# Optimization experiments

Hardware: AMD Instinct MI355X
Metric: run time of the kernel (lower is better)

Reference implementation:

```python
import jax, jax.numpy as jnp
import numpy as np

B = 4096      # batch
D_IN = 512    # input_dim
D = 256       # d_model
T = 424       # n_targets
L = 6         # num_layers
EPS = 1e-5    # torch LayerNorm default


def _ln(x, g, b):
    m = jnp.mean(x, axis=-1, keepdims=True)
    v = jnp.var(x, axis=-1, keepdims=True)
    return (x - m) * jax.lax.rsqrt(v + EPS) * g + b


def setup_inputs() -> dict:
    key = jax.random.key(0)
    ks = iter(jax.random.split(key, 32))
    r = lambda shape, s=0.05: jax.random.normal(next(ks), shape, dtype=jnp.float32) * s
    return {
        'x': jax.random.normal(next(ks), (B, D_IN), dtype=jnp.float32),
        'proj_W': r((4, D // 4, D_IN)), 'proj_b': r((4, D // 4)),
        'attn_in_W': r((L, 3 * D, D)), 'attn_in_b': r((L, 3 * D)),
        'attn_out_W': r((L, D, D)), 'attn_out_b': r((L, D)),
        'ln_g': jnp.ones((L, D), jnp.float32), 'ln_b': jnp.zeros((L, D), jnp.float32),
        'ff_W1': r((L, 4 * D, D)), 'ff_b1': r((L, 4 * D)),
        'ff_W2': r((L, D, 4 * D)), 'ff_b2': r((L, D)),
        'cross_in_W': r((3 * D, D)), 'cross_in_b': r((3 * D,)),
        'cross_out_W': r((D, D)), 'cross_out_b': r((D,)),
        'tp_W1': r((T, D // 2, D)), 'tp_b1': r((T, D // 2)),
        'tp_ln_g': jnp.ones((T, D // 2), jnp.float32), 'tp_ln_b': jnp.zeros((T, D // 2), jnp.float32),
        'tp_W2': r((T, D // 4, D // 2)), 'tp_b2': r((T, D // 4)),
        'tp_W3': r((T, D // 4)), 'tp_b3': r((T,)),
    }


def reference(x, proj_W, proj_b, attn_in_W, attn_in_b, attn_out_W, attn_out_b,
              ln_g, ln_b, ff_W1, ff_b1, ff_W2, ff_b2,
              cross_in_W, cross_in_b, cross_out_W, cross_out_b,
              tp_W1, tp_b1, tp_ln_g, tp_ln_b, tp_W2, tp_b2, tp_W3, tp_b3):
    # 4 feature projections -> concat == reshape of stacked einsum  [B, 4, D/4] -> [B, D]
    h = jnp.einsum('bd,pkd->bpk', x, proj_W) + proj_b
    h = h.reshape(h.shape[0], D)

    # 6 transformer blocks on seq_len=1: softmax over a single key == 1, so
    # MHA(x,x,x) reduces exactly to out_proj(v_proj(x)); dropout = identity (eval).
    for i in range(L):
        Wv, bv = attn_in_W[i, 2 * D:], attn_in_b[i, 2 * D:]
        attn = (h @ Wv.T + bv) @ attn_out_W[i].T + attn_out_b[i]
        h = _ln(h + attn, ln_g[i], ln_b[i])          # same norm instance reused
        ff = jax.nn.gelu(h @ ff_W1[i].T + ff_b1[i], approximate=False) @ ff_W2[i].T + ff_b2[i]
        h = _ln(h + ff, ln_g[i], ln_b[i])

    # cross-target attention, also seq_len=1 -> v/out projections only
    Wv, bv = cross_in_W[2 * D:], cross_in_b[2 * D:]
    h = h + ((h @ Wv.T + bv) @ cross_out_W.T + cross_out_b)

    # 424 per-target MLP heads, batched as grouped GEMMs
    t = jnp.einsum('bd,tkd->btk', h, tp_W1) + tp_b1          # [B, T, 128]
    t = jax.nn.relu(_ln(t, tp_ln_g, tp_ln_b))
    t = jax.nn.relu(jnp.einsum('btk,tmk->btm', t, tp_W2) + tp_b2)  # [B, T, 64]
    out = jnp.einsum('btm,tm->bt', t, tp_W3) + tp_b3         # [B, T]
    return out
```

## Files before the change

### kernel.cpp

```cpp
#include <hip/hip_runtime.h>
#include <stdint.h>

using bf16x8 = __attribute__((ext_vector_type(8))) short;
using f32x4  = __attribute__((ext_vector_type(4))) float;

__device__ __forceinline__ f32x4 mfma16(bf16x8 a, bf16x8 b, f32x4 c) {
  return __builtin_amdgcn_mfma_f32_16x16x32_bf16(a, b, c, 0, 0, 0);
}

__device__ __forceinline__ unsigned short f2b_rne(float f) {
  union { float f; unsigned u; } v; v.f = f;
  unsigned r = v.u + 0x7fffu + ((v.u >> 16) & 1u);
  return (unsigned short)(r >> 16);
}

__global__ void f2b_kernel(const float* __restrict__ s, unsigned short* __restrict__ d, int n4) {
  int i = blockIdx.x * 256 + threadIdx.x;
  if (i >= n4) return;
  float4 v = reinterpret_cast<const float4*>(s)[i];
  ushort4 o;
  o.x = f2b_rne(v.x); o.y = f2b_rne(v.y); o.z = f2b_rne(v.z); o.w = f2b_rne(v.w);
  reinterpret_cast<ushort4*>(d)[i] = o;
}

__global__ __launch_bounds__(256) void compose_attn(
    const float* __restrict__ aiW, const float* __restrict__ aib,
    const float* __restrict__ aoW, const float* __restrict__ aob,
    const float* __restrict__ ciW, const float* __restrict__ cib,
    const float* __restrict__ coW, const float* __restrict__ cob,
    unsigned short* __restrict__ wEff, float* __restrict__ bEff) {
  const int mat = blockIdx.y;
  const float* Wo = (mat < 6) ? aoW + (size_t)mat * 65536 : coW;
  const float* Wv = (mat < 6) ? aiW + (size_t)mat * 196608 + 131072 : ciW + 131072;
  const float* bv = (mat < 6) ? aib + mat * 768 + 512 : cib + 512;
  const float* bo = (mat < 6) ? aob + mat * 256 : cob;
  unsigned short* Wd = wEff + (size_t)mat * 65536;
  const int m = blockIdx.x * 16 + (threadIdx.x >> 4);
  const int k0 = (threadIdx.x & 15) * 16;
  float c[16] = {};
  for (int j = 0; j < 256; ++j) {
    const float a = Wo[m * 256 + j];
    const float* Br = Wv + j * 256 + k0;
#pragma unroll
    for (int kk = 0; kk < 16; ++kk) c[kk] = fmaf(a, Br[kk], c[kk]);
  }
#pragma unroll
  for (int kk = 0; kk < 16; ++kk) Wd[m * 256 + k0 + kk] = f2b_rne(c[kk]);
  if (blockIdx.x == 0) {
    const int mm = threadIdx.x;
    float s = 0.f;
    for (int j = 0; j < 256; ++j) s = fmaf(Wo[mm * 256 + j], bv[j], s);
    bEff[mat * 256 + mm] = s + bo[mm];
  }
}

template<int NCF, int K, int NK>
__device__ __forceinline__ void gemm_ws(const unsigned short* __restrict__ Wb,
                                        const char* __restrict__ smA_r,
                                        int hi16, int swz, f32x4 (&acc)[NCF]) {
  bf16x8 w[3][NCF];
#pragma unroll
  for (int p = 0; p < 2; ++p)
#pragma unroll
    for (int cf = 0; cf < NCF; ++cf)
      w[p][cf] = *reinterpret_cast<const bf16x8*>(Wb + (size_t)cf * 16 * K + p * 32);
#pragma unroll
  for (int ks = 0; ks < NK; ++ks) {
    const bf16x8 a = *reinterpret_cast<const bf16x8*>(smA_r + ((ks * 64 + hi16) ^ swz));
    if (ks + 2 < NK) {
#pragma unroll
      for (int cf = 0; cf < NCF; ++cf)
        w[(ks + 2) % 3][cf] = *reinterpret_cast<const bf16x8*>(Wb + (size_t)cf * 16 * K + (ks + 2) * 32);
    }
#pragma unroll
    for (int cf = 0; cf < NCF; ++cf)
      acc[cf] = mfma16(a, w[ks % 3][cf], acc[cf]);
  }
}

__global__ __launch_bounds__(512, 2) void trunk_fused(
    const unsigned short* __restrict__ xb, const unsigned short* __restrict__ pWb,
    const float* __restrict__ projb,
    const unsigned short* __restrict__ wEff, const float* __restrict__ bEff,
    const unsigned short* __restrict__ f1Wb, const float* __restrict__ f1b,
    const unsigned short* __restrict__ f2Wb, const float* __restrict__ f2bp,
    const float* __restrict__ lng, const float* __restrict__ lnb,
    unsigned short* __restrict__ hbf) {
  __shared__ char hbuf[16 * 512];
  __shared__ char gbuf[16 * 2048];
  __shared__ float red[2][16][8];
  const int tid = threadIdx.x, wid = tid >> 6, lane = tid & 63;
  const int r = lane & 15, hi = lane >> 4;
  const int swz = (r & 7) << 4, hi16 = hi * 16;
  const int row0 = blockIdx.x << 4;
  const int colb = wid * 32;

#pragma unroll
  for (int i = 0; i < 2; ++i) {
    const int id = tid + i * 512, row = id >> 6, c8 = id & 63;
    bf16x8 v = *reinterpret_cast<const bf16x8*>(xb + (size_t)(row0 + row) * 512 + c8 * 8);
    *reinterpret_cast<bf16x8*>(gbuf + row * 1024 + ((c8 * 16) ^ ((row & 7) << 4))) = v;
  }
  __syncthreads();

  f32x4 hreg[2];

  auto store_hb = [&]() {
#pragma unroll
    for (int cf = 0; cf < 2; ++cf) {
      const int cb = (colb + cf * 16 + r) * 2;
#pragma unroll
      for (int j = 0; j < 4; ++j) {
        const int row = hi * 4 + j;
        *reinterpret_cast<unsigned short*>(hbuf + row * 512 + (cb ^ ((row & 7) << 4))) =
            f2b_rne(hreg[cf][j]);
      }
    }
  };

  auto ln_apply = [&](float gm0, float gm1, float bb0, float bb1) {
    float sum[4], sq[4];
#pragma unroll
    for (int j = 0; j < 4; ++j) {
      const float v0 = hreg[0][j], v1 = hreg[1][j];
      sum[j] = v0 + v1; sq[j] = v0 * v0 + v1 * v1;
    }
#pragma unroll
    for (int m = 1; m < 16; m <<= 1)
#pragma unroll
      for (int j = 0; j < 4; ++j) {
        sum[j] += __shfl_xor(sum[j], m, 64);
        sq[j]  += __shfl_xor(sq[j],  m, 64);
      }
    if (r == 0)
#pragma unroll
      for (int j = 0; j < 4; ++j) {
        red[0][hi * 4 + j][wid] = sum[j];
        red[1][hi * 4 + j][wid] = sq[j];
      }
    __syncthreads();
#pragma unroll
    for (int j = 0; j < 4; ++j) {
      const int row = hi * 4 + j;
      f32x4 p0 = *reinterpret_cast<const f32x4*>(&red[0][row][0]);
      f32x4 p1 = *reinterpret_cast<const f32x4*>(&red[0][row][4]);
      f32x4 q0 = *reinterpret_cast<const f32x4*>(&red[1][row][0]);
      f32x4 q1 = *reinterpret_cast<const f32x4*>(&red[1][row][4]);
      const float ts = p0[0]+p0[1]+p0[2]+p0[3]+p1[0]+p1[1]+p1[2]+p1[3];
      const float tq = q0[0]+q0[1]+q0[2]+q0[3]+q1[0]+q1[1]+q1[2]+q1[3];
      const float mean = ts * (1.f / 256.f);
      const float rstd = rsqrtf(tq * (1.f / 256.f) - mean * mean + 1e-5f);
      hreg[0][j] = (hreg[0][j] - mean) * rstd * gm0 + bb0;
      hreg[1][j] = (hreg[1][j] - mean) * rstd * gm1 + bb1;
    }
  };

  {
    f32x4 acc[2] = {};
    gemm_ws<2, 512, 16>(pWb + (size_t)(colb + r) * 512 + hi * 8, gbuf + r * 1024, hi16, swz, acc);
    const float bv0 = projb[colb + r], bv1 = projb[colb + 16 + r];
#pragma unroll
    for (int j = 0; j < 4; ++j) { hreg[0][j] = acc[0][j] + bv0; hreg[1][j] = acc[1][j] + bv1; }
  }
  store_hb();
  __syncthreads();

  for (int L = 0; L < 6; ++L) {
    const float gm0 = lng[L * 256 + colb + r],      gm1 = lng[L * 256 + colb + 16 + r];
    const float bb0 = lnb[L * 256 + colb + r],      bb1 = lnb[L * 256 + colb + 16 + r];
    {
      f32x4 acc[2] = {};
      gemm_ws<2, 256, 8>(wEff + (size_t)L * 65536 + (size_t)(colb + r) * 256 + hi * 8,
                         hbuf + r * 512, hi16, swz, acc);
      const float be0 = bEff[L * 256 + colb + r], be1 = bEff[L * 256 + colb + 16 + r];
#pragma unroll
      for (int j = 0; j < 4; ++j) { hreg[0][j] += acc[0][j] + be0; hreg[1][j] += acc[1][j] + be1; }
    }
    ln_apply(gm0, gm1, bb0, bb1);
    store_hb();
    __syncthreads();
    {
      f32x4 accf[8] = {};
      gemm_ws<8, 256, 8>(f1Wb + (size_t)L * 262144 + (size_t)(wid * 128 + r) * 256 + hi * 8,
                         hbuf + r * 512, hi16, swz, accf);
#pragma unroll
      for (int cf = 0; cf < 8; ++cf) {
        const int colw = wid * 128 + cf * 16 + r;
        const float bv = f1b[L * 1024 + colw];
        const int cb = colw * 2;
#pragma unroll
        for (int j = 0; j < 4; ++j) {
          float y = accf[cf][j] + bv;
          y = 0.5f * y * (1.f + erff(y * 0.70710678118654752f));
          const int row = hi * 4 + j;
          *reinterpret_cast<unsigned short*>(gbuf + row * 2048 + (cb ^ ((row & 7) << 4))) = f2b_rne(y);
        }
      }
    }
    __syncthreads();
    {
      f32x4 acc[2] = {};
      gemm_ws<2, 1024, 32>(f2Wb + (size_t)L * 262144 + (size_t)(colb + r) * 1024 + hi * 8,
                           gbuf + r * 2048, hi16, swz, acc);
      const float be0 = f2bp[L * 256 + colb + r], be1 = f2bp[L * 256 + colb + 16 + r];
#pragma unroll
      for (int j = 0; j < 4; ++j) { hreg[0][j] += acc[0][j] + be0; hreg[1][j] += acc[1][j] + be1; }
    }
    ln_apply(gm0, gm1, bb0, bb1);
    store_hb();
    __syncthreads();
  }

  {
    f32x4 acc[2] = {};
    gemm_ws<2, 256, 8>(wEff + 6ull * 65536 + (size_t)(colb + r) * 256 + hi * 8,
                       hbuf + r * 512, hi16, swz, acc);
    const float be0 = bEff[1536 + colb + r], be1 = bEff[1536 + colb + 16 + r];
#pragma unroll
    for (int j = 0; j < 4; ++j) { hreg[0][j] += acc[0][j] + be0; hreg[1][j] += acc[1][j] + be1; }
  }
#pragma unroll
  for (int cf = 0; cf < 2; ++cf)
#pragma unroll
    for (int j = 0; j < 4; ++j)
      hbf[(size_t)(row0 + hi * 4 + j) * 256 + colb + cf * 16 + r] = f2b_rne(hreg[cf][j]);
}

__global__ __launch_bounds__(512, 2) void phase_d2(
    const unsigned short* __restrict__ hbf, const unsigned short* __restrict__ w1b,
    const float* __restrict__ b1, const float* __restrict__ lng, const float* __restrict__ lnb,
    const unsigned short* __restrict__ w2b, const float* __restrict__ b2,
    const float* __restrict__ w3, const float* __restrict__ b3,
    float* __restrict__ out) {
  __shared__ char sm[149504];
  const int tid = threadIdx.x, wid = tid >> 6, lane = tid & 63;
  const int r = lane & 15, hi = lane >> 4;
  const int sw = (r & 7) << 4;
  const int t = blockIdx.y;

  const unsigned short* w1t = w1b + (size_t)t * 32768;
  const unsigned short* w2t = w2b + (size_t)t * 8192;
#pragma unroll
  for (int i = 0; i < 8; ++i) {
    const int id = tid + i * 512;
    const int c = id >> 5, s = id & 31;
    bf16x8 v = *reinterpret_cast<const bf16x8*>(w1t + c * 256 + s * 8);
    *reinterpret_cast<bf16x8*>(sm + c * 512 + ((s * 16) ^ ((c & 7) << 4))) = v;
  }
#pragma unroll
  for (int i = 0; i < 2; ++i) {
    const int id = tid + i * 512;
    const int c = id >> 4, s = id & 15;
    bf16x8 v = *reinterpret_cast<const bf16x8*>(w2t + c * 128 + s * 8);
    *reinterpret_cast<bf16x8*>(sm + 65536 + c * 256 + ((s * 16) ^ ((c & 7) << 4))) = v;
  }
  {
    float v;
    if (tid < 128)      v = b1 [t * 128 + tid];
    else if (tid < 256) v = lng[t * 128 + tid - 128];
    else if (tid < 384) v = lnb[t * 128 + tid - 256];
    else if (tid < 448) v = b2 [t * 64  + tid - 384];
    else                v = w3 [t * 64  + tid - 448];
    reinterpret_cast<float*>(sm + 81920)[tid] = v;
  }
  __syncthreads();

  const float* cb1 = reinterpret_cast<const float*>(sm + 81920);
  const float* cg  = cb1 + 128;
  const float* cbe = cb1 + 256;
  const float* cb2 = cb1 + 384;
  const float* cw3 = cb1 + 448;
  char* t1w = sm + 83968 + wid * 8192;
  const float b3t = b3[t];
  const int token_b0 = blockIdx.x * 1024;

  for (int tile = 0; tile < 2; ++tile) {
    const int B0 = token_b0 + tile * 512 + wid * 64;

    f32x4 acc1[8][4] = {};
    bf16x8 bc[4], bn[4];
#pragma unroll
    for (int bf = 0; bf < 4; ++bf)
      bc[bf] = *reinterpret_cast<const bf16x8*>(hbf + (size_t)(B0 + bf * 16 + r) * 256 + hi * 8);
#pragma unroll
    for (int ks = 0; ks < 8; ++ks) {
      bf16x8 a[8];
#pragma unroll
      for (int cf = 0; cf < 8; ++cf)
        a[cf] = *reinterpret_cast<const bf16x8*>(sm + (cf * 16 + r) * 512 + ((ks * 64 + hi * 16) ^ sw));
      if (ks < 7) {
#pragma unroll
        for (int bf = 0; bf < 4; ++bf)
          bn[bf] = *reinterpret_cast<const bf16x8*>(hbf + (size_t)(B0 + bf * 16 + r) * 256 + (ks + 1) * 32 + hi * 8);
      }
#pragma unroll
      for (int cf = 0; cf < 8; ++cf)
#pragma unroll
        for (int bf = 0; bf < 4; ++bf)
          acc1[cf][bf] = mfma16(a[cf], bc[bf], acc1[cf][bf]);
#pragma unroll
      for (int bf = 0; bf < 4; ++bf) bc[bf] = bn[bf];
    }

#pragma unroll
    for (int cf = 0; cf < 8; ++cf) {
      f32x4 b1v = *reinterpret_cast<const f32x4*>(cb1 + cf * 16 + hi * 4);
#pragma unroll
      for (int bf = 0; bf < 4; ++bf) acc1[cf][bf] += b1v;
    }

    float mu[4], rsd[4];
#pragma unroll
    for (int bf = 0; bf < 4; ++bf) {
      float s = 0.f, s2 = 0.f;
#pragma unroll
      for (int cf = 0; cf < 8; ++cf)
#pragma unroll
        for (int j = 0; j < 4; ++j) { float v = acc1[cf][bf][j]; s += v; s2 += v * v; }
      s  += __shfl_xor(s, 16, 64);  s  += __shfl_xor(s, 32, 64);
      s2 += __shfl_xor(s2, 16, 64); s2 += __shfl_xor(s2, 32, 64);
      const float m = s * (1.f / 128.f);
      mu[bf] = m;
      rsd[bf] = rsqrtf(s2 * (1.f / 128.f) - m * m + 1e-5f);
    }

    f32x4 acc2[4][4] = {};
#pragma unroll
    for (int half = 0; half < 2; ++half) {
#pragma unroll
      for (int cf = 0; cf < 8; ++cf) {
        f32x4 gv = *reinterpret_cast<const f32x4*>(cg  + cf * 16 + hi * 4);
        f32x4 bv = *reinterpret_cast<const f32x4*>(cbe + cf * 16 + hi * 4);
#pragma unroll
        for (int bl = 0; bl < 2; ++bl) {
          const int bf = half * 2 + bl;
          unsigned o01, o23;
          {
            float y0 = fmaxf((acc1[cf][bf][0] - mu[bf]) * rsd[bf] * gv[0] + bv[0], 0.f);
            float y1 = fmaxf((acc1[cf][bf][1] - mu[bf]) * rsd[bf] * gv[1] + bv[1], 0.f);
            float y2 = fmaxf((acc1[cf][bf][2] - mu[bf]) * rsd[bf] * gv[2] + bv[2], 0.f);
            float y3 = fmaxf((acc1[cf][bf][3] - mu[bf]) * rsd[bf] * gv[3] + bv[3], 0.f);
            o01 = (unsigned)f2b_rne(y0) | ((unsigned)f2b_rne(y1) << 16);
            o23 = (unsigned)f2b_rne(y2) | ((unsigned)f2b_rne(y3) << 16);
          }
          uint2 pk; pk.x = o01; pk.y = o23;
          *reinterpret_cast<uint2*>(t1w + (bl * 16 + r) * 256 + ((cf * 32 + hi * 8) ^ sw)) = pk;
        }
      }
#pragma unroll
      for (int ks = 0; ks < 4; ++ks) {
        bf16x8 a2[4];
#pragma unroll
        for (int cf2 = 0; cf2 < 4; ++cf2)
          a2[cf2] = *reinterpret_cast<const bf16x8*>(sm + 65536 + (cf2 * 16 + r) * 256 + ((ks * 64 + hi * 16) ^ sw));
#pragma unroll
        for (int bl = 0; bl < 2; ++bl) {
          bf16x8 bb = *reinterpret_cast<const bf16x8*>(t1w + (bl * 16 + r) * 256 + ((ks * 64 + hi * 16) ^ sw));
#pragma unroll
          for (int cf2 = 0; cf2 < 4; ++cf2)
            acc2[cf2][half * 2 + bl] = mfma16(a2[cf2], bb, acc2[cf2][half * 2 + bl]);
        }
      }
    }

    float s[4] = {0.f, 0.f, 0.f, 0.f};
#pragma unroll
    for (int cf2 = 0; cf2 < 4; ++cf2) {
      f32x4 b2v = *reinterpret_cast<const f32x4*>(cb2 + cf2 * 16 + hi * 4);
      f32x4 w3v = *reinterpret_cast<const f32x4*>(cw3 + cf2 * 16 + hi * 4);
#pragma unroll
      for (int bf = 0; bf < 4; ++bf)
#pragma unroll
        for (int j = 0; j < 4; ++j)
          s[bf] += fmaxf(acc2[cf2][bf][j] + b2v[j], 0.f) * w3v[j];
    }
#pragma unroll
    for (int bf = 0; bf < 4; ++bf) {
      s[bf] += __shfl_xor(s[bf], 16, 64);
      s[bf] += __shfl_xor(s[bf], 32, 64);
      if (hi == 0) out[(size_t)(B0 + bf * 16 + r) * 424 + t] = s[bf] + b3t;
    }
  }
}

extern "C" void kernel_launch(void* const* d_in, const int* in_sizes, int n_in,
                              void* d_out, int out_size, void* d_ws, size_t ws_size,
                              hipStream_t stream) {
  const float* x     = (const float*)d_in[0];
  const float* projW = (const float*)d_in[1];
  const float* projb = (const float*)d_in[2];
  const float* aiW   = (const float*)d_in[3];
  const float* aib   = (const float*)d_in[4];
  const float* aoW   = (const float*)d_in[5];
  const float* aob   = (const float*)d_in[6];
  const float* lng   = (const float*)d_in[7];
  const float* lnbp  = (const float*)d_in[8];
  const float* f1W   = (const float*)d_in[9];
  const float* f1b   = (const float*)d_in[10];
  const float* f2W   = (const float*)d_in[11];
  const float* f2bp  = (const float*)d_in[12];
  const float* ciW   = (const float*)d_in[13];
  const float* cib   = (const float*)d_in[14];
  const float* coW   = (const float*)d_in[15];
  const float* cob   = (const float*)d_in[16];
  const float* tpW1  = (const float*)d_in[17];
  const float* tpb1  = (const float*)d_in[18];
  const float* tplng = (const float*)d_in[19];
  const float* tplnb = (const float*)d_in[20];
  const float* tpW2  = (const float*)d_in[21];
  const float* tpb2  = (const float*)d_in[22];
  const float* tpW3  = (const float*)d_in[23];
  const float* tpb3  = (const float*)d_in[24];
  float* out = (float*)d_out;

  char* ws = (char*)d_ws;
  size_t off = 0;
  auto alloc = [&](size_t n) { char* p = ws + off; off = (off + n + 255) & ~(size_t)255; return p; };
  unsigned short* xb   = (unsigned short*)alloc(4096ull * 512 * 2);
  unsigned short* pWb  = (unsigned short*)alloc(256ull * 512 * 2);
  unsigned short* f1Wb = (unsigned short*)alloc(6ull * 1024 * 256 * 2);
  unsigned short* f2Wb = (unsigned short*)alloc(6ull * 256 * 1024 * 2);
  unsigned short* W1b  = (unsigned short*)alloc(424ull * 128 * 256 * 2);
  unsigned short* W2b  = (unsigned short*)alloc(424ull * 64 * 128 * 2);
  unsigned short* wEff = (unsigned short*)alloc(7ull * 256 * 256 * 2);
  float*          bEff = (float*)alloc(7ull * 256 * 4);
  unsigned short* hbf  = (unsigned short*)alloc(4096ull * 256 * 2);

  auto conv = [&](const float* s, unsigned short* d, size_t n) {
    int n4 = (int)(n >> 2);
    f2b_kernel<<<dim3((n4 + 255) / 256), dim3(256), 0, stream>>>(s, d, n4);
  };
  compose_attn<<<dim3(16, 7), dim3(256), 0, stream>>>(aiW, aib, aoW, aob, ciW, cib, coW, cob, wEff, bEff);
  conv(x, xb, 4096ull * 512);
  conv(projW, pWb, 256ull * 512);
  conv(f1W, f1Wb, 6ull * 1024 * 256);
  conv(f2W, f2Wb, 6ull * 256 * 1024);
  conv(tpW1, W1b, 424ull * 128 * 256);
  conv(tpW2, W2b, 424ull * 64 * 128);

  trunk_fused<<<dim3(256), dim3(512), 0, stream>>>(
      xb, pWb, projb, wEff, bEff, f1Wb, f1b, f2Wb, f2bp, lng, lnbp, hbf);

  phase_d2<<<dim3(4, 424), dim3(512), 0, stream>>>(hbf, W1b, tpb1, tplng, tplnb, W2b, tpb2, tpW3, tpb3, out);
}
```

Measured before the change: 559.1 us.

## Stream trunk GEMM weights through per-wave LDS ring with async global-to-LDS loads

Replaces the register-prefetched weight loads in the trunk GEMMs with a per-wave, three-slot LDS ring. Each slot holds a swizzled 16x128 bf16 tile, filled by asynchronous global_load_lds. Tiles are issued two steps ahead and gated with explicit vmcnt waits, so weight fetches overlap MFMA work and register pressure drops. The cost is a 96KB shared ring, which brings the trunk kernel's LDS use to roughly 137KB per block. That likely prevents the two blocks per CU that the launch bounds request.

```diff
diff --git a/kernel.cpp b/kernel.cpp
--- a/kernel.cpp
+++ b/kernel.cpp
@@ -1,5 +1,7 @@
 #include <hip/hip_runtime.h>
 #include <stdint.h>
+#include <utility>
+#include <type_traits>
 
 using bf16x8 = __attribute__((ext_vector_type(8))) short;
 using f32x4  = __attribute__((ext_vector_type(4))) float;
@@ -12,6 +14,73 @@
   union { float f; unsigned u; } v; v.f = f;
   unsigned r = v.u + 0x7fffu + ((v.u >> 16) & 1u);
   return (unsigned short)(r >> 16);
+}
+
+__device__ __forceinline__ void gload16(const void* g, void* l) {
+  __builtin_amdgcn_global_load_lds(
+      (const __attribute__((address_space(1))) void*)g,
+      (__attribute__((address_space(3))) void*)l, 16, 0, 0);
+}
+
+template<int N> __device__ __forceinline__ void vmwait() {
+  if constexpr (N <= 0)      asm volatile("s_waitcnt vmcnt(0)" ::: "memory");
+  else if constexpr (N == 4) asm volatile("s_waitcnt vmcnt(4)" ::: "memory");
+  else                       asm volatile("s_waitcnt vmcnt(8)" ::: "memory");
+}
+
+template<class F, int... Is>
+__device__ __forceinline__ void sfor_impl(F&& f, std::integer_sequence<int, Is...>) {
+  (f(std::integral_constant<int, Is>{}), ...);
+}
+template<int N, class F>
+__device__ __forceinline__ void sfor(F&& f) {
+  sfor_impl(static_cast<F&&>(f), std::make_integer_sequence<int, N>{});
+}
+
+__device__ __forceinline__ void stage_tile(const unsigned short* __restrict__ W, int K,
+                                           int col0, int kt, char* slot, int lane) {
+#pragma unroll
+  for (int i = 0; i < 4; ++i) {
+    const int chunk = i * 64 + lane;
+    const int ci = chunk >> 4, kc = chunk & 15;
+    const unsigned short* src = W + (size_t)(col0 + ci) * K + kt * 128
+                                + (((kc * 16) ^ ((ci & 7) << 4)) >> 1);
+    gload16(src, slot + i * 1024);
+  }
+}
+
+template<int NCG, int NKT, int AS, int K>
+__device__ __forceinline__ void gemm_pipe(const unsigned short* __restrict__ W, int c0,
+                                          const char* __restrict__ abuf,
+                                          char* __restrict__ ring, int lane,
+                                          f32x4 (&acc)[NCG]) {
+  const int r = lane & 15, hi16 = (lane >> 4) << 4;
+  const int swz = (r & 7) << 4;
+  constexpr int TILES = NCG * NKT;
+  stage_tile(W, K, c0, 0, ring, lane);
+  if constexpr (TILES > 1)
+    stage_tile(W, K, c0 + (1 % NCG) * 16, 1 / NCG, ring + 4096, lane);
+  bf16x8 areg[4];
+  sfor<TILES>([&](auto tc) {
+    constexpr int t = tc.value;
+    constexpr int kt = t / NCG, cg = t % NCG;
+    vmwait<((t + 2 <= TILES) ? 4 : 0)>();
+    __builtin_amdgcn_sched_barrier(0);
+    if constexpr (t + 2 < TILES) {
+      constexpr int t2 = t + 2;
+      stage_tile(W, K, c0 + (t2 % NCG) * 16, t2 / NCG, ring + (t2 % 3) * 4096, lane);
+    }
+    const char* slot = ring + (t % 3) * 4096;
+#pragma unroll
+    for (int ksl = 0; ksl < 4; ++ksl) {
+      if constexpr (cg == 0)
+        areg[ksl] = *reinterpret_cast<const bf16x8*>(
+            abuf + r * AS + ((kt * 256 + ksl * 64 + hi16) ^ swz));
+      const bf16x8 b = *reinterpret_cast<const bf16x8*>(
+          slot + r * 256 + ((ksl * 64 + hi16) ^ swz));
+      acc[cg] = mfma16(areg[ksl], b, acc[cg]);
+    }
+  });
 }
 
 __global__ void f2b_kernel(const float* __restrict__ s, unsigned short* __restrict__ d, int n4) {
@@ -54,30 +123,6 @@
   }
 }
 
-template<int NCF, int K, int NK>
-__device__ __forceinline__ void gemm_ws(const unsigned short* __restrict__ Wb,
-                                        const char* __restrict__ smA_r,
-                                        int hi16, int swz, f32x4 (&acc)[NCF]) {
-  bf16x8 w[3][NCF];
-#pragma unroll
-  for (int p = 0; p < 2; ++p)
-#pragma unroll
-    for (int cf = 0; cf < NCF; ++cf)
-      w[p][cf] = *reinterpret_cast<const bf16x8*>(Wb + (size_t)cf * 16 * K + p * 32);
-#pragma unroll
-  for (int ks = 0; ks < NK; ++ks) {
-    const bf16x8 a = *reinterpret_cast<const bf16x8*>(smA_r + ((ks * 64 + hi16) ^ swz));
-    if (ks + 2 < NK) {
-#pragma unroll
-      for (int cf = 0; cf < NCF; ++cf)
-        w[(ks + 2) % 3][cf] = *reinterpret_cast<const bf16x8*>(Wb + (size_t)cf * 16 * K + (ks + 2) * 32);
-    }
-#pragma unroll
-    for (int cf = 0; cf < NCF; ++cf)
-      acc[cf] = mfma16(a, w[ks % 3][cf], acc[cf]);
-  }
-}
-
 __global__ __launch_bounds__(512, 2) void trunk_fused(
     const unsigned short* __restrict__ xb, const unsigned short* __restrict__ pWb,
     const float* __restrict__ projb,
@@ -88,12 +133,14 @@
     unsigned short* __restrict__ hbf) {
   __shared__ char hbuf[16 * 512];
   __shared__ char gbuf[16 * 2048];
+  __shared__ char ringbuf[8 * 12288];
   __shared__ float red[2][16][8];
   const int tid = threadIdx.x, wid = tid >> 6, lane = tid & 63;
   const int r = lane & 15, hi = lane >> 4;
-  const int swz = (r & 7) << 4, hi16 = hi * 16;
+  const int swz = (r & 7) << 4;
   const int row0 = blockIdx.x << 4;
   const int colb = wid * 32;
+  char* ring = ringbuf + wid * 12288;
 
 #pragma unroll
   for (int i = 0; i < 2; ++i) {
@@ -157,7 +204,7 @@
 
   {
     f32x4 acc[2] = {};
-    gemm_ws<2, 512, 16>(pWb + (size_t)(colb + r) * 512 + hi * 8, gbuf + r * 1024, hi16, swz, acc);
+    gemm_pipe<2, 4, 1024, 512>(pWb, colb, gbuf, ring, lane, acc);
     const float bv0 = projb[colb + r], bv1 = projb[colb + 16 + r];
 #pragma unroll
     for (int j = 0; j < 4; ++j) { hreg[0][j] = acc[0][j] + bv0; hreg[1][j] = acc[1][j] + bv1; }
@@ -170,8 +217,7 @@
     const float bb0 = lnb[L * 256 + colb + r],      bb1 = lnb[L * 256 + colb + 16 + r];
     {
       f32x4 acc[2] = {};
-      gemm_ws<2, 256, 8>(wEff + (size_t)L * 65536 + (size_t)(colb + r) * 256 + hi * 8,
-                         hbuf + r * 512, hi16, swz, acc);
+      gemm_pipe<2, 2, 512, 256>(wEff + (size_t)L * 65536, colb, hbuf, ring, lane, acc);
       const float be0 = bEff[L * 256 + colb + r], be1 = bEff[L * 256 + colb + 16 + r];
 #pragma unroll
       for (int j = 0; j < 4; ++j) { hreg[0][j] += acc[0][j] + be0; hreg[1][j] += acc[1][j] + be1; }
@@ -181,8 +227,7 @@
     __syncthreads();
     {
       f32x4 accf[8] = {};
-      gemm_ws<8, 256, 8>(f1Wb + (size_t)L * 262144 + (size_t)(wid * 128 + r) * 256 + hi * 8,
-                         hbuf + r * 512, hi16, swz, accf);
+      gemm_pipe<8, 2, 512, 256>(f1Wb + (size_t)L * 262144, wid * 128, hbuf, ring, lane, accf);
 #pragma unroll
       for (int cf = 0; cf < 8; ++cf) {
         const int colw = wid * 128 + cf * 16 + r;
@@ -200,8 +245,7 @@
     __syncthreads();
     {
       f32x4 acc[2] = {};
-      gemm_ws<2, 1024, 32>(f2Wb + (size_t)L * 262144 + (size_t)(colb + r) * 1024 + hi * 8,
-                           gbuf + r * 2048, hi16, swz, acc);
+      gemm_pipe<2, 8, 2048, 1024>(f2Wb + (size_t)L * 262144, colb, gbuf, ring, lane, acc);
       const float be0 = f2bp[L * 256 + colb + r], be1 = f2bp[L * 256 + colb + 16 + r];
 #pragma unroll
       for (int j = 0; j < 4; ++j) { hreg[0][j] += acc[0][j] + be0; hreg[1][j] += acc[1][j] + be1; }
@@ -213,8 +257,7 @@
 
   {
     f32x4 acc[2] = {};
-    gemm_ws<2, 256, 8>(wEff + 6ull * 65536 + (size_t)(colb + r) * 256 + hi * 8,
-                       hbuf + r * 512, hi16, swz, acc);
+    gemm_pipe<2, 2, 512, 256>(wEff + 6ull * 65536, colb, hbuf, ring, lane, acc);
     const float be0 = bEff[1536 + colb + r], be1 = bEff[1536 + colb + 16 + r];
 #pragma unroll
     for (int j = 0; j < 4; ++j) { hreg[0][j] += acc[0][j] + be0; hreg[1][j] += acc[1][j] + be1; }
```

Result: faster. 523.6 us (-6.3%).
